# Kernel optimization log

Hardware: AMD Instinct MI355X
Metric: run time of the kernel (lower is better)

The kernel has to match this reference:

```python
import jax, jax.numpy as jnp
import numpy as np

C_IN = 32
C_OUT = 32


def setup_inputs() -> dict:
    key = jax.random.key(0)
    k1, k2, k3 = jax.random.split(key, 3)
    B, N, P_DIM = 32, 4096, 64
    X = jax.random.normal(k1, (B, N, C_IN), dtype=jnp.float32)
    P = jax.random.normal(k2, (B, N, P_DIM), dtype=jnp.float32)
    # glorot-ish scale for the hypernetwork Dense kernel (p_dim -> c_in*c_out)
    scale = (2.0 / (P_DIM + C_IN * C_OUT)) ** 0.5
    Wk = jax.random.normal(k3, (P_DIM, C_IN * C_OUT), dtype=jnp.float32) * scale
    return {"X": X, "P": P, "Wk": Wk}


def reference(X, P, Wk):
    B, N, c_in = X.shape
    # hypernetwork: per-position weight generation  [B,N,p] @ [p, c_in*c_out]
    A = jnp.einsum('bnp,pq->bnq', P, Wk)
    W = A.reshape(B, N, c_in, C_OUT)          # [B,N,c_in,c_out]
    W = jax.nn.relu(W)                        # sigma(W)
    # batched per-position GEMV: y_bno = sum_i X_bni * W_bnio
    out = jnp.einsum('bni,bnio->bno', X, W)   # [B,N,c_out]
    return out
```

## Files before the change

### kernel.cpp

```cpp
#include <hip/hip_runtime.h>

#define CI 32
#define CO 32
#define PD 64
#define QDIM 1024
#define M_TOTAL (32*4096)
#define TILE_M 128
#define NBLK (M_TOTAL/TILE_M)
#define WG_THREADS 256
#define XLS 33
#define OLS 33

typedef float  f32x4  __attribute__((ext_vector_type(4)));
typedef float  f32x16 __attribute__((ext_vector_type(16)));
typedef __bf16 bf16x4 __attribute__((ext_vector_type(4)));
typedef __bf16 bf16x8 __attribute__((ext_vector_type(8)));

__global__ __launch_bounds__(256)
void wk_pack_kernel(const float* __restrict__ Wk, __bf16* __restrict__ wsF)
{
    __shared__ float tile[64][33];
    const int q0 = blockIdx.x * 32;
    const int t  = threadIdx.x;
#pragma unroll
    for (int s = 0; s < 2; ++s) {
        const int idx = t + s * 256;
        const int k = idx >> 3, ch = idx & 7;
        f32x4 v = *(const f32x4*)(Wk + (size_t)k * QDIM + q0 + ch * 4);
        tile[k][ch*4+0] = v[0]; tile[k][ch*4+1] = v[1];
        tile[k][ch*4+2] = v[2]; tile[k][ch*4+3] = v[3];
    }
    __syncthreads();
    const int qq = t >> 3;
    const int g  = t & 7;
    bf16x8 o;
#pragma unroll
    for (int j = 0; j < 8; ++j) o[j] = (__bf16)tile[g*8 + j][qq];
    *(bf16x8*)(wsF + (size_t)blockIdx.x * 2048 + g * 256 + qq * 8) = o;
}

__global__ __launch_bounds__(WG_THREADS, 2)
void cond_dense_kernel(const float* __restrict__ Xg, const float* __restrict__ Pg,
                       const __bf16* __restrict__ wsF, float* __restrict__ outg)
{
    __shared__ union {
        __bf16 p[TILE_M * PD];
        float  o[2 * 64 * OLS];
    } U;
    __shared__ float Xl[TILE_M * XLS];

    const int t   = threadIdx.x;
    const int l   = t & 63;
    const int w   = t >> 6;
    const int rg  = w & 1;
    const int ih  = w >> 1;
    const int l31 = l & 31;
    const int hi  = l >> 5;
    const int tile0 = blockIdx.x * TILE_M;
    const int m0  = rg * 64 + l31;

    {
        const float* Pb = Pg + (size_t)tile0 * PD;
#pragma unroll
        for (int s = 0; s < 8; ++s) {
            const int id = t + 256 * s;
            const int r = id >> 4, ch = id & 15;
            f32x4 v = *(const f32x4*)(Pb + (size_t)r * PD + ch * 4);
            bf16x4 bv;
#pragma unroll
            for (int j = 0; j < 4; ++j) bv[j] = (__bf16)v[j];
            char* dst = (char*)U.p + r * 128
                      + ((((ch >> 1) ^ (r & 7)) << 4) | ((ch & 1) * 8));
            *(bf16x4*)dst = bv;
        }
        const float* Xb = Xg + (size_t)tile0 * CI;
#pragma unroll
        for (int s = 0; s < 4; ++s) {
            const int id = t + 256 * s;
            const int r = id >> 3, ch = id & 7;
            f32x4 v = *(const f32x4*)(Xb + (size_t)r * CI + ch * 4);
#pragma unroll
            for (int j = 0; j < 4; ++j) Xl[r * XLS + ch * 4 + j] = v[j];
        }
    }
    __syncthreads();

    bf16x8 bfA[4], bfB[4];
#pragma unroll
    for (int kq = 0; kq < 4; ++kq) {
        const int g = ((kq * 2 + hi) ^ (l31 & 7)) << 4;
        bfA[kq] = *(const bf16x8*)((const char*)U.p + m0 * 128 + g);
        bfB[kq] = *(const bf16x8*)((const char*)U.p + (m0 + 32) * 128 + g);
    }

    f32x16 oA = {}, oB = {};
    const __bf16* abase = wsF + (size_t)(ih * 16) * 2048
                        + (size_t)hi * 256 + (size_t)l31 * 8;
    const float* xb0 = &Xl[m0 * XLS + ih * 16];
    const float* xb1 = &Xl[(m0 + 32) * XLS + ih * 16];

    bf16x8 a0[4], a1[4];
    auto aload = [&](int i, bf16x8* buf) {
        const __bf16* ap = abase + (size_t)i * 2048;
        buf[0] = *(const bf16x8*)(ap);
        buf[1] = *(const bf16x8*)(ap +  512);
        buf[2] = *(const bf16x8*)(ap + 1024);
        buf[3] = *(const bf16x8*)(ap + 1536);
    };
    auto step = [&](const bf16x8* a, int i) {
        const float xl = xb0[i];
        const float xh = xb1[i];
        f32x16 c0 = {}, c1 = {};
#pragma unroll
        for (int kq = 0; kq < 4; ++kq) {
            c0 = __builtin_amdgcn_mfma_f32_32x32x16_bf16(a[kq], bfA[kq], c0, 0, 0, 0);
            c1 = __builtin_amdgcn_mfma_f32_32x32x16_bf16(a[kq], bfB[kq], c1, 0, 0, 0);
        }
#pragma unroll
        for (int r = 0; r < 16; ++r) {
            oA[r] += fmaxf(c0[r], 0.0f) * xl;
            oB[r] += fmaxf(c1[r], 0.0f) * xh;
        }
    };

    aload(0, a0);
    aload(1, a1);
    for (int ii = 0; ii < 8; ++ii) {
        step(a0, 2 * ii);
        if (ii < 7) aload(2 * ii + 2, a0);
        step(a1, 2 * ii + 1);
        if (ii < 7) aload(2 * ii + 3, a1);
    }

    __syncthreads();
    if (ih == 1) {
        const int ob = (rg * 64 + l) * OLS;
#pragma unroll
        for (int r = 0; r < 16; ++r) {
            U.o[ob + r]      = oA[r];
            U.o[ob + 16 + r] = oB[r];
        }
    }
    __syncthreads();
    if (ih == 0) {
        const int ob = (rg * 64 + l) * OLS;
#pragma unroll
        for (int r = 0; r < 16; ++r) {
            oA[r] += U.o[ob + r];
            oB[r] += U.o[ob + 16 + r];
        }
        float* orow  = outg + (size_t)(tile0 + m0) * CO + 4 * hi;
        float* orow2 = orow + 32 * CO;
#pragma unroll
        for (int rq = 0; rq < 4; ++rq) {
            f32x4 vA, vB;
#pragma unroll
            for (int j = 0; j < 4; ++j) { vA[j] = oA[4*rq + j]; vB[j] = oB[4*rq + j]; }
            *(f32x4*)(orow  + 8 * rq) = vA;
            *(f32x4*)(orow2 + 8 * rq) = vB;
        }
    }
}

extern "C" void kernel_launch(void* const* d_in, const int* in_sizes, int n_in,
                              void* d_out, int out_size, void* d_ws, size_t ws_size,
                              hipStream_t stream)
{
    const float* X  = (const float*)d_in[0];
    const float* P  = (const float*)d_in[1];
    const float* Wk = (const float*)d_in[2];
    float* out  = (float*)d_out;
    __bf16* wsF = (__bf16*)d_ws;

    wk_pack_kernel<<<dim3(QDIM / 32), dim3(256), 0, stream>>>(Wk, wsF);
    cond_dense_kernel<<<dim3(NBLK), dim3(WG_THREADS), 0, stream>>>(X, P, wsF, out);
}
```

Measured before the change: 36.68 us.

## Switch hypernetwork GEMM to 16x16x32 MFMA with packed-f32x2 relu-scale epilogue

Replaces the 32x32x16 bf16 MFMA tiling with 16x16x32 MFMA tiles, repacking the Wk workspace layout and the P fragment loads to match. The relu-times-x accumulation now runs on f32x2 vectors, so the compiler can emit packed FP32 ops, and the main loop is fully unrolled. The aim is fewer epilogue VALU instructions and better MFMA/VALU interleaving. In exchange it adds more MFMA issues per tile and changes the register pressure profile.

```diff
diff --git a/kernel.cpp b/kernel.cpp
--- a/kernel.cpp
+++ b/kernel.cpp
@@ -11,16 +11,17 @@
 #define XLS 33
 #define OLS 33
 
+typedef float  f32x2  __attribute__((ext_vector_type(2)));
 typedef float  f32x4  __attribute__((ext_vector_type(4)));
-typedef float  f32x16 __attribute__((ext_vector_type(16)));
 typedef __bf16 bf16x4 __attribute__((ext_vector_type(4)));
 typedef __bf16 bf16x8 __attribute__((ext_vector_type(8)));
 
 __global__ __launch_bounds__(256)
-void wk_pack_kernel(const float* __restrict__ Wk, __bf16* __restrict__ wsF)
+void wk_pack16(const float* __restrict__ Wk, __bf16* __restrict__ wsG)
 {
     __shared__ float tile[64][33];
-    const int q0 = blockIdx.x * 32;
+    const int i  = blockIdx.x;
+    const int q0 = i * 32;
     const int t  = threadIdx.x;
 #pragma unroll
     for (int s = 0; s < 2; ++s) {
@@ -32,16 +33,19 @@
     }
     __syncthreads();
     const int qq = t >> 3;
-    const int g  = t & 7;
+    const int g8 = t & 7;
+    const int kh = g8 >> 2, g = g8 & 3;
+    const int qb = qq >> 4, c = qq & 15;
     bf16x8 o;
 #pragma unroll
-    for (int j = 0; j < 8; ++j) o[j] = (__bf16)tile[g*8 + j][qq];
-    *(bf16x8*)(wsF + (size_t)blockIdx.x * 2048 + g * 256 + qq * 8) = o;
+    for (int j = 0; j < 8; ++j) o[j] = (__bf16)tile[kh*32 + g*8 + j][qq];
+    *(bf16x8*)((char*)wsG + (size_t)i * 4096 + qb * 2048 + kh * 1024
+               + g * 256 + c * 16) = o;
 }
 
 __global__ __launch_bounds__(WG_THREADS, 2)
 void cond_dense_kernel(const float* __restrict__ Xg, const float* __restrict__ Pg,
-                       const __bf16* __restrict__ wsF, float* __restrict__ outg)
+                       const __bf16* __restrict__ wsG, float* __restrict__ outg)
 {
     __shared__ union {
         __bf16 p[TILE_M * PD];
@@ -54,10 +58,10 @@
     const int w   = t >> 6;
     const int rg  = w & 1;
     const int ih  = w >> 1;
-    const int l31 = l & 31;
-    const int hi  = l >> 5;
+    const int c16 = l & 15;
+    const int h4  = l >> 4;
     const int tile0 = blockIdx.x * TILE_M;
-    const int m0  = rg * 64 + l31;
+    const int mbase = rg * 64;
 
     {
         const float* Pb = Pg + (size_t)tile0 * PD;
@@ -85,79 +89,93 @@
     }
     __syncthreads();
 
-    bf16x8 bfA[4], bfB[4];
+    bf16x8 bfr[4][2];
 #pragma unroll
-    for (int kq = 0; kq < 4; ++kq) {
-        const int g = ((kq * 2 + hi) ^ (l31 & 7)) << 4;
-        bfA[kq] = *(const bf16x8*)((const char*)U.p + m0 * 128 + g);
-        bfB[kq] = *(const bf16x8*)((const char*)U.p + (m0 + 32) * 128 + g);
+    for (int mq = 0; mq < 4; ++mq) {
+        const int row = mbase + mq * 16 + c16;
+#pragma unroll
+        for (int kh = 0; kh < 2; ++kh) {
+            const int g = ((h4 + 4 * kh) ^ (row & 7)) << 4;
+            bfr[mq][kh] = *(const bf16x8*)((const char*)U.p + row * 128 + g);
+        }
     }
 
-    f32x16 oA = {}, oB = {};
-    const __bf16* abase = wsF + (size_t)(ih * 16) * 2048
-                        + (size_t)hi * 256 + (size_t)l31 * 8;
-    const float* xb0 = &Xl[m0 * XLS + ih * 16];
-    const float* xb1 = &Xl[(m0 + 32) * XLS + ih * 16];
+    f32x2 oacc[16] = {};
+    const char* abase = (const char*)wsG + (size_t)(ih * 16) * 4096
+                      + h4 * 256 + c16 * 16;
+    const float* xb = &Xl[(mbase + c16) * XLS + ih * 16];
 
-    bf16x8 a0[4], a1[4];
-    auto aload = [&](int i, bf16x8* buf) {
-        const __bf16* ap = abase + (size_t)i * 2048;
-        buf[0] = *(const bf16x8*)(ap);
-        buf[1] = *(const bf16x8*)(ap +  512);
-        buf[2] = *(const bf16x8*)(ap + 1024);
-        buf[3] = *(const bf16x8*)(ap + 1536);
+    bf16x8 aq[4], an[4];
+    auto aload = [&](int il, bf16x8* buf) {
+        const char* p = abase + (size_t)il * 4096;
+        buf[0] = *(const bf16x8*)(p);
+        buf[1] = *(const bf16x8*)(p + 1024);
+        buf[2] = *(const bf16x8*)(p + 2048);
+        buf[3] = *(const bf16x8*)(p + 3072);
     };
-    auto step = [&](const bf16x8* a, int i) {
-        const float xl = xb0[i];
-        const float xh = xb1[i];
-        f32x16 c0 = {}, c1 = {};
+    const f32x2 zero2 = {0.0f, 0.0f};
+    auto step = [&](const bf16x8* a, int il) {
+        f32x2 x2[4];
 #pragma unroll
-        for (int kq = 0; kq < 4; ++kq) {
-            c0 = __builtin_amdgcn_mfma_f32_32x32x16_bf16(a[kq], bfA[kq], c0, 0, 0, 0);
-            c1 = __builtin_amdgcn_mfma_f32_32x32x16_bf16(a[kq], bfB[kq], c1, 0, 0, 0);
+        for (int mq = 0; mq < 4; ++mq) {
+            const float x = xb[mq * 16 * XLS + il];
+            x2[mq][0] = x; x2[mq][1] = x;
         }
 #pragma unroll
-        for (int r = 0; r < 16; ++r) {
-            oA[r] += fmaxf(c0[r], 0.0f) * xl;
-            oB[r] += fmaxf(c1[r], 0.0f) * xh;
+        for (int qb = 0; qb < 2; ++qb) {
+            f32x4 cc[4] = {};
+#pragma unroll
+            for (int mq = 0; mq < 4; ++mq) {
+                cc[mq] = __builtin_amdgcn_mfma_f32_16x16x32_bf16(a[qb*2+0], bfr[mq][0], cc[mq], 0, 0, 0);
+                cc[mq] = __builtin_amdgcn_mfma_f32_16x16x32_bf16(a[qb*2+1], bfr[mq][1], cc[mq], 0, 0, 0);
+            }
+#pragma unroll
+            for (int mq = 0; mq < 4; ++mq) {
+#pragma unroll
+                for (int p = 0; p < 2; ++p) {
+                    f32x2 pr = {cc[mq][2*p], cc[mq][2*p + 1]};
+                    oacc[qb*8 + mq*2 + p] +=
+                        __builtin_elementwise_max(pr, zero2) * x2[mq];
+                }
+            }
         }
     };
 
-    aload(0, a0);
-    aload(1, a1);
+    aload(0, aq);
+    aload(1, an);
+#pragma unroll
     for (int ii = 0; ii < 8; ++ii) {
-        step(a0, 2 * ii);
-        if (ii < 7) aload(2 * ii + 2, a0);
-        step(a1, 2 * ii + 1);
-        if (ii < 7) aload(2 * ii + 3, a1);
+        step(aq, 2 * ii);
+        if (ii < 7) aload(2 * ii + 2, aq);
+        step(an, 2 * ii + 1);
+        if (ii < 7) aload(2 * ii + 3, an);
     }
 
     __syncthreads();
+    const int ob = (rg * 64 + l) * OLS;
     if (ih == 1) {
-        const int ob = (rg * 64 + l) * OLS;
 #pragma unroll
-        for (int r = 0; r < 16; ++r) {
-            U.o[ob + r]      = oA[r];
-            U.o[ob + 16 + r] = oB[r];
-        }
+        for (int r = 0; r < 16; ++r)
+            *(f32x2*)&U.o[ob + 2*r] = oacc[r];
     }
     __syncthreads();
     if (ih == 0) {
-        const int ob = (rg * 64 + l) * OLS;
 #pragma unroll
-        for (int r = 0; r < 16; ++r) {
-            oA[r] += U.o[ob + r];
-            oB[r] += U.o[ob + 16 + r];
-        }
-        float* orow  = outg + (size_t)(tile0 + m0) * CO + 4 * hi;
-        float* orow2 = orow + 32 * CO;
+        for (int r = 0; r < 16; ++r)
+            oacc[r] += *(const f32x2*)&U.o[ob + 2*r];
 #pragma unroll
-        for (int rq = 0; rq < 4; ++rq) {
-            f32x4 vA, vB;
+        for (int qb = 0; qb < 2; ++qb) {
 #pragma unroll
-            for (int j = 0; j < 4; ++j) { vA[j] = oA[4*rq + j]; vB[j] = oB[4*rq + j]; }
-            *(f32x4*)(orow  + 8 * rq) = vA;
-            *(f32x4*)(orow2 + 8 * rq) = vB;
+            for (int mq = 0; mq < 4; ++mq) {
+                f32x4 v;
+                v[0] = oacc[qb*8 + mq*2 + 0][0];
+                v[1] = oacc[qb*8 + mq*2 + 0][1];
+                v[2] = oacc[qb*8 + mq*2 + 1][0];
+                v[3] = oacc[qb*8 + mq*2 + 1][1];
+                float* orow = outg + (size_t)(tile0 + mbase + mq*16 + c16) * CO
+                            + qb * 16 + h4 * 4;
+                *(f32x4*)orow = v;
+            }
         }
     }
 }
@@ -170,8 +188,8 @@
     const float* P  = (const float*)d_in[1];
     const float* Wk = (const float*)d_in[2];
     float* out  = (float*)d_out;
-    __bf16* wsF = (__bf16*)d_ws;
+    __bf16* wsG = (__bf16*)d_ws;
 
-    wk_pack_kernel<<<dim3(QDIM / 32), dim3(256), 0, stream>>>(Wk, wsF);
-    cond_dense_kernel<<<dim3(NBLK), dim3(WG_THREADS), 0, stream>>>(X, P, wsF, out);
+    wk_pack16<<<dim3(CI), dim3(256), 0, stream>>>(Wk, wsG);
+    cond_dense_kernel<<<dim3(NBLK), dim3(WG_THREADS), 0, stream>>>(X, P, wsG, out);
 }
```

After: 36.29 us (median of 2 runs). About the same (-1.1%).
